# Kernel tuning notes

Measured on AMD Instinct MI355X. Metric: run time of the kernel, lower is better.

The kernel has to match this reference:

```python
import jax, jax.numpy as jnp
import numpy as np

KEEP_RATIO = 0.5
B, H, W = 8, 1024, 1024


def setup_inputs() -> dict:
    key = jax.random.key(0)
    k1, k2, k3 = jax.random.split(key, 3)
    logits = jax.random.normal(k1, (B, 1, H, W), dtype=jnp.float32)
    targets = jax.random.randint(k2, (B, 1, H, W), 0, 2, dtype=jnp.int32)
    tissue_mask = jax.random.randint(k3, (B, 1, H, W), 0, 2, dtype=jnp.int32)
    return {"logits": logits, "targets": targets, "tissue_mask": tissue_mask}


def reference(logits, targets, tissue_mask):
    b = logits.shape[0]
    x = logits.reshape(b, -1)                       # (B, N)
    t = targets.reshape(b, -1).astype(x.dtype)      # {0,1}
    m = tissue_mask.reshape(b, -1).astype(x.dtype)  # {0,1}
    n = x.shape[1]

    # stable binary_cross_entropy_with_logits, reduction='none'
    bce = jnp.maximum(x, 0.0) - x * t + jnp.log1p(jnp.exp(-jnp.abs(x)))
    loss = bce * m                                  # masked per-pixel loss

    pos = t * m                                     # positives inside tissue
    neg = (1.0 - t) * m                             # negatives inside tissue
    n_pos = jnp.sum(pos, axis=1)                    # (B,)
    n_neg = jnp.sum(neg, axis=1)

    k_all = max(1, int(n * KEEP_RATIO))             # static python int
    # kept count per row: all positives + top-(k_all - n_pos) negatives (clamped)
    k_keep = n_pos + jnp.minimum(jnp.maximum(k_all - n_pos, 0.0), n_neg)  # (B,)

    BIG = jnp.asarray(1e30, x.dtype)
    # sort key: positives always first, then negatives by loss, then non-tissue
    sort_key = jnp.where(pos > 0, BIG, jnp.where(neg > 0, loss, -BIG))
    order = jnp.argsort(-sort_key, axis=1)          # descending
    sorted_loss = jnp.take_along_axis(loss, order, axis=1)

    ranks = jnp.arange(n, dtype=x.dtype)
    keep = (ranks[None, :] < k_keep[:, None]).astype(x.dtype)
    per_sample = jnp.sum(sorted_loss * keep, axis=1) / jnp.maximum(k_keep, 1.0)
    # fallback when no tissue pixels at all: torch keeps index 0 (loss there is 0)
    per_sample = jnp.where(k_keep > 0, per_sample, loss[:, 0])
    return jnp.mean(per_sample)
```

## Files before the change

### kernel.cpp

```cpp
#include <hip/hip_runtime.h>
#include <cstdint>
#include <cstddef>

#define N_PIX   1048576
#define B_ROWS  8
#define K_ALL   524288
#define BLOCKS_PER_ROW 128
#define NSTAGE  8
#define NBINS   1024
#define FXSHIFT 11
#define NCOPY   8
#define CSHIFT  42
#define SUMMASK ((1ull << CSHIFT) - 1ull)
#define FPSCALE 262144.0f


__global__ __launch_bounds__(256) void k_pass1(
    const float4* __restrict__ lg, const int4* __restrict__ tg, const int4* __restrict__ mk,
    unsigned long long* __restrict__ hist,
    unsigned* __restrict__ partNpos, double* __restrict__ partSpos, float* __restrict__ out)
{
    __shared__ unsigned long long hq[NBINS];
    __shared__ unsigned swp[4];
    __shared__ double   sws[4];
    const int tid = threadIdx.x;

    for (int b = tid; b < NBINS; b += 256) hq[b] = 0ull;
    if (blockIdx.x == 0 && tid == 0) *out = 0.f;
    __syncthreads();
    __builtin_amdgcn_sched_barrier(0);

    const int r = blockIdx.x >> 7;
    const size_t qbase = (size_t)blockIdx.x * (NSTAGE * 256) + tid;

    unsigned npos = 0; float spos = 0.f;

    auto proc = [&](float xx, int tt, int mm) {
        float ax = fabsf(xx);
        float e = __expf(-ax);
        float l = __logf(1.f + e);
        float bce = fmaxf(xx, 0.f) - xx * (float)tt + l;
        if (mm) {
            if (tt) { npos++; spos += bce; }
            else {
                unsigned fx = (unsigned)__float2uint_rn(bce * FPSCALE);
                unsigned bin = fx >> FXSHIFT;
                if (bin >= NBINS) bin = NBINS - 1;
                atomicAdd(&hq[bin], (1ull << CSHIFT) | (unsigned long long)fx);
            }
        }
    };

    float4 x[2]; int4 t[2]; int4 m[2];
    x[0] = lg[qbase]; t[0] = tg[qbase]; m[0] = mk[qbase];
    #pragma unroll
    for (int j = 0; j < NSTAGE; ++j) {
        const int cur = j & 1, nxt = cur ^ 1;
        if (j < NSTAGE - 1) {
            const size_t q = qbase + (size_t)(j + 1) * 256;
            x[nxt] = lg[q]; t[nxt] = tg[q]; m[nxt] = mk[q];
        }
        __builtin_amdgcn_sched_barrier(0);
        proc(x[cur].x, t[cur].x, m[cur].x);
        proc(x[cur].y, t[cur].y, m[cur].y);
        proc(x[cur].z, t[cur].z, m[cur].z);
        proc(x[cur].w, t[cur].w, m[cur].w);
        __builtin_amdgcn_sched_barrier(0);
    }

    for (int o = 32; o; o >>= 1) {
        npos += __shfl_down(npos, o);
        spos += __shfl_down(spos, o);
    }
    if ((tid & 63) == 0) { swp[tid >> 6] = npos; sws[tid >> 6] = (double)spos; }
    __syncthreads();
    if (tid == 0) {
        partNpos[blockIdx.x] = swp[0] + swp[1] + swp[2] + swp[3];
        partSpos[blockIdx.x] = sws[0] + sws[1] + sws[2] + sws[3];
    }

    unsigned long long* gh = hist + ((size_t)r * NCOPY + (blockIdx.x & (NCOPY - 1))) * NBINS;
    for (int b = tid; b < NBINS; b += 256) {
        unsigned long long v = hq[b];
        if (v) atomicAdd(&gh[b], v);
    }
}

__global__ __launch_bounds__(256) void k_final(
    const unsigned long long* __restrict__ hist,
    const unsigned* __restrict__ partNpos, const double* __restrict__ partSpos,
    float* __restrict__ out)
{
    __shared__ unsigned sc[2][256];
    __shared__ double   sd[2][256];
    __shared__ unsigned swp[4];
    __shared__ double   sws[4];
    __shared__ unsigned rcntgt, rcnt1;
    __shared__ double rsumgt, rsum1;

    const int r = blockIdx.x, tid = threadIdx.x;
    const unsigned long long* gh = hist + (size_t)r * NCOPY * NBINS;
    const double inv = 1.0 / (double)FPSCALE;

    {
        unsigned np = (tid < BLOCKS_PER_ROW) ? partNpos[r * BLOCKS_PER_ROW + tid] : 0u;
        double   sp = (tid < BLOCKS_PER_ROW) ? partSpos[r * BLOCKS_PER_ROW + tid] : 0.0;
        for (int o = 32; o; o >>= 1) { np += __shfl_down(np, o); sp += __shfl_down(sp, o); }
        if ((tid & 63) == 0) { swp[tid >> 6] = np; sws[tid >> 6] = sp; }
    }
    __syncthreads();
    const unsigned npos = swp[0] + swp[1] + swp[2] + swp[3];
    const double sumPos = sws[0] + sws[1] + sws[2] + sws[3];
    __syncthreads();

    const int per = NBINS / 256;
    const int b0 = NBINS - 1 - tid * per;
    unsigned lc[4]; double lsum[4];
    unsigned pc = 0; double ps = 0.0;
    #pragma unroll
    for (int i = 0; i < per; ++i) {
        unsigned long long v = 0ull;
        #pragma unroll
        for (int c = 0; c < NCOPY; ++c) v += gh[(size_t)c * NBINS + (b0 - i)];
        lc[i] = (unsigned)(v >> CSHIFT);
        lsum[i] = (double)(v & SUMMASK) * inv;
        pc += lc[i]; ps += lsum[i];
    }

    int pp = 0;
    sc[0][tid] = pc; sd[0][tid] = ps;
    __syncthreads();
    for (int ofs = 1; ofs < 256; ofs <<= 1) {
        unsigned c = sc[pp][tid]; double s = sd[pp][tid];
        if (tid >= ofs) { c += sc[pp][tid - ofs]; s += sd[pp][tid - ofs]; }
        sc[pp ^ 1][tid] = c; sd[pp ^ 1][tid] = s;
        pp ^= 1;
        __syncthreads();
    }
    const unsigned nneg   = sc[pp][255];
    const double   sumNeg = sd[pp][255];

    long kl = (long)K_ALL - (long)npos;
    if (kl < 0) kl = 0;
    if (kl > (long)nneg) kl = (long)nneg;
    const unsigned Kneg = (unsigned)kl;

    double sum_sel = 0.0;
    if (Kneg >= nneg) {
        sum_sel = sumNeg;
    } else if (Kneg > 0) {
        unsigned inc = sc[pp][tid];
        unsigned exc = inc - pc;
        double   exs = sd[pp][tid] - ps;
        if (exc < Kneg && Kneg <= inc) {
            unsigned cum = exc; double csum = exs;
            #pragma unroll
            for (int i = 0; i < per; ++i) {
                if (cum + lc[i] >= Kneg) {
                    rcntgt = cum; rsumgt = csum;
                    rcnt1 = lc[i]; rsum1 = lsum[i];
                    break;
                }
                cum += lc[i]; csum += lsum[i];
            }
        }
        __syncthreads();
        if (tid == 0) {
            const unsigned cntT1 = rcnt1;
            const double   sumT1 = rsum1;
            const unsigned Kp = Kneg - rcntgt;
            const double w = 1.0 / 128.0;
            const double avg = sumT1 / (double)cntT1;
            const double topmean = avg + 0.5 * w * (1.0 - (double)Kp / (double)cntT1);
            sum_sel = rsumgt + (double)Kp * topmean;
        }
    }

    if (tid == 0) {
        unsigned long long kk = (unsigned long long)npos + (unsigned long long)Kneg;
        double per_s = 0.0;
        if (kk > 0) per_s = (sumPos + sum_sel) / (double)kk;
        atomicAdd(out, (float)(per_s / (double)B_ROWS));
    }
}

extern "C" void kernel_launch(void* const* d_in, const int* in_sizes, int n_in,
                              void* d_out, int out_size, void* d_ws, size_t ws_size,
                              hipStream_t stream)
{
    const float* logits = (const float*)d_in[0];
    const int*   targets = (const int*)d_in[1];
    const int*   tissue = (const int*)d_in[2];

    const int NBLK = B_ROWS * BLOCKS_PER_ROW;
    char* ws = (char*)d_ws;
    size_t off = 0;
    unsigned long long* hist = (unsigned long long*)(ws + off);
    off += (size_t)B_ROWS * NCOPY * NBINS * 8;
    size_t zero_size = off;
    unsigned* partNpos = (unsigned*)(ws + off); off += (size_t)NBLK * 4;
    double*   partSpos = (double*)(ws + off);   off += (size_t)NBLK * 8;

    hipMemsetAsync(ws, 0, zero_size, stream);

    k_pass1<<<NBLK, 256, 0, stream>>>(
        (const float4*)logits, (const int4*)targets, (const int4*)tissue,
        hist, partNpos, partSpos, (float*)d_out);
    k_final<<<B_ROWS, 256, 0, stream>>>(hist, partNpos, partSpos, (float*)d_out);
}
```

Measured before the change: 121.5 us.

## Split loss and histogram into separate kernels via packed 16-bit fixed-point buffer

The fused pass is split in two. One kernel computes BCE and writes each negative pixel's loss as a 16-bit fixed-point value (others get a sentinel), packed two per word, into a workspace buffer. A second kernel reads these values and builds the per-row shared-memory histogram with 64-bit atomics, then merges it into the global histogram copies. This separates the bandwidth-bound transcendental pass from the atomic-heavy histogram pass to raise occupancy in each, at the cost of an extra 16 MB write and read. Fixed-point precision also drops from a 2^18 to a 2^13 scale, with losses clamped at 0xFFFE, which coarsens the top-k boundary interpolation.

```diff
diff --git a/kernel.cpp b/kernel.cpp
--- a/kernel.cpp
+++ b/kernel.cpp
@@ -5,67 +5,63 @@
 #define N_PIX   1048576
 #define B_ROWS  8
 #define K_ALL   524288
-#define BLOCKS_PER_ROW 128
-#define NSTAGE  8
+#define LOSS_BLOCKS 2048
+#define LOSS_STAGES 4
+#define HIST_BLOCKS 1024
+#define HPT     4
 #define NBINS   1024
-#define FXSHIFT 11
 #define NCOPY   8
 #define CSHIFT  42
 #define SUMMASK ((1ull << CSHIFT) - 1ull)
-#define FPSCALE 262144.0f
-
-
-__global__ __launch_bounds__(256) void k_pass1(
+#define FXSCALE 8192.0f
+
+
+__global__ __launch_bounds__(256) void k_loss(
     const float4* __restrict__ lg, const int4* __restrict__ tg, const int4* __restrict__ mk,
-    unsigned long long* __restrict__ hist,
+    uint4* __restrict__ fxout,
     unsigned* __restrict__ partNpos, double* __restrict__ partSpos, float* __restrict__ out)
 {
-    __shared__ unsigned long long hq[NBINS];
     __shared__ unsigned swp[4];
     __shared__ double   sws[4];
     const int tid = threadIdx.x;
-
-    for (int b = tid; b < NBINS; b += 256) hq[b] = 0ull;
     if (blockIdx.x == 0 && tid == 0) *out = 0.f;
-    __syncthreads();
-    __builtin_amdgcn_sched_barrier(0);
-
-    const int r = blockIdx.x >> 7;
-    const size_t qbase = (size_t)blockIdx.x * (NSTAGE * 256) + tid;
+
+    const size_t qbase = (size_t)blockIdx.x * (LOSS_STAGES * 256) + tid;
 
     unsigned npos = 0; float spos = 0.f;
 
-    auto proc = [&](float xx, int tt, int mm) {
+    auto bcefx = [&](float xx, int tt, int mm) -> unsigned {
         float ax = fabsf(xx);
         float e = __expf(-ax);
         float l = __logf(1.f + e);
         float bce = fmaxf(xx, 0.f) - xx * (float)tt + l;
-        if (mm) {
-            if (tt) { npos++; spos += bce; }
-            else {
-                unsigned fx = (unsigned)__float2uint_rn(bce * FPSCALE);
-                unsigned bin = fx >> FXSHIFT;
-                if (bin >= NBINS) bin = NBINS - 1;
-                atomicAdd(&hq[bin], (1ull << CSHIFT) | (unsigned long long)fx);
-            }
-        }
+        unsigned fx = __float2uint_rn(bce * FXSCALE);
+        if (fx > 0xFFFEu) fx = 0xFFFEu;
+        if (mm && tt) { npos++; spos += bce; }
+        return (mm && !tt) ? fx : 0xFFFFu;
     };
 
     float4 x[2]; int4 t[2]; int4 m[2];
     x[0] = lg[qbase]; t[0] = tg[qbase]; m[0] = mk[qbase];
-    #pragma unroll
-    for (int j = 0; j < NSTAGE; ++j) {
+    uint4 acc;
+    #pragma unroll
+    for (int j = 0; j < LOSS_STAGES; ++j) {
         const int cur = j & 1, nxt = cur ^ 1;
-        if (j < NSTAGE - 1) {
+        if (j < LOSS_STAGES - 1) {
             const size_t q = qbase + (size_t)(j + 1) * 256;
             x[nxt] = lg[q]; t[nxt] = tg[q]; m[nxt] = mk[q];
         }
         __builtin_amdgcn_sched_barrier(0);
-        proc(x[cur].x, t[cur].x, m[cur].x);
-        proc(x[cur].y, t[cur].y, m[cur].y);
-        proc(x[cur].z, t[cur].z, m[cur].z);
-        proc(x[cur].w, t[cur].w, m[cur].w);
-        __builtin_amdgcn_sched_barrier(0);
+        unsigned f0 = bcefx(x[cur].x, t[cur].x, m[cur].x);
+        unsigned f1 = bcefx(x[cur].y, t[cur].y, m[cur].y);
+        unsigned f2 = bcefx(x[cur].z, t[cur].z, m[cur].z);
+        unsigned f3 = bcefx(x[cur].w, t[cur].w, m[cur].w);
+        if ((j & 1) == 0) {
+            acc.x = f0 | (f1 << 16); acc.y = f2 | (f3 << 16);
+        } else {
+            acc.z = f0 | (f1 << 16); acc.w = f2 | (f3 << 16);
+            fxout[(size_t)blockIdx.x * (2 * 256) + (size_t)(j >> 1) * 256 + tid] = acc;
+        }
     }
 
     for (int o = 32; o; o >>= 1) {
@@ -78,11 +74,41 @@
         partNpos[blockIdx.x] = swp[0] + swp[1] + swp[2] + swp[3];
         partSpos[blockIdx.x] = sws[0] + sws[1] + sws[2] + sws[3];
     }
+}
+
+__global__ __launch_bounds__(256) void k_hist(
+    const uint4* __restrict__ fx4, unsigned long long* __restrict__ hist)
+{
+    __shared__ unsigned long long hq[NBINS];
+    const int tid = threadIdx.x;
+    for (int b = tid; b < NBINS; b += 256) hq[b] = 0ull;
+    __syncthreads();
+
+    const int r = blockIdx.x >> 7;
+    const size_t base = (size_t)blockIdx.x * (HPT * 256) + tid;
+
+    uint4 v[HPT];
+    #pragma unroll
+    for (int s = 0; s < HPT; ++s) v[s] = fx4[base + (size_t)s * 256];
+
+    #pragma unroll
+    for (int s = 0; s < HPT; ++s) {
+        unsigned w[4] = { v[s].x, v[s].y, v[s].z, v[s].w };
+        #pragma unroll
+        for (int q = 0; q < 4; ++q) {
+            unsigned lo = w[q] & 0xFFFFu, hi = w[q] >> 16;
+            if (lo != 0xFFFFu)
+                atomicAdd(&hq[lo >> 6], (1ull << CSHIFT) | (unsigned long long)lo);
+            if (hi != 0xFFFFu)
+                atomicAdd(&hq[hi >> 6], (1ull << CSHIFT) | (unsigned long long)hi);
+        }
+    }
+    __syncthreads();
 
     unsigned long long* gh = hist + ((size_t)r * NCOPY + (blockIdx.x & (NCOPY - 1))) * NBINS;
     for (int b = tid; b < NBINS; b += 256) {
-        unsigned long long v = hq[b];
-        if (v) atomicAdd(&gh[b], v);
+        unsigned long long u = hq[b];
+        if (u) atomicAdd(&gh[b], u);
     }
 }
 
@@ -100,11 +126,11 @@
 
     const int r = blockIdx.x, tid = threadIdx.x;
     const unsigned long long* gh = hist + (size_t)r * NCOPY * NBINS;
-    const double inv = 1.0 / (double)FPSCALE;
+    const double inv = 1.0 / (double)FXSCALE;
 
     {
-        unsigned np = (tid < BLOCKS_PER_ROW) ? partNpos[r * BLOCKS_PER_ROW + tid] : 0u;
-        double   sp = (tid < BLOCKS_PER_ROW) ? partSpos[r * BLOCKS_PER_ROW + tid] : 0.0;
+        unsigned np = partNpos[r * 256 + tid];
+        double   sp = partSpos[r * 256 + tid];
         for (int o = 32; o; o >>= 1) { np += __shfl_down(np, o); sp += __shfl_down(sp, o); }
         if ((tid & 63) == 0) { swp[tid >> 6] = np; sws[tid >> 6] = sp; }
     }
@@ -192,19 +218,20 @@
     const int*   targets = (const int*)d_in[1];
     const int*   tissue = (const int*)d_in[2];
 
-    const int NBLK = B_ROWS * BLOCKS_PER_ROW;
     char* ws = (char*)d_ws;
     size_t off = 0;
     unsigned long long* hist = (unsigned long long*)(ws + off);
     off += (size_t)B_ROWS * NCOPY * NBINS * 8;
     size_t zero_size = off;
-    unsigned* partNpos = (unsigned*)(ws + off); off += (size_t)NBLK * 4;
-    double*   partSpos = (double*)(ws + off);   off += (size_t)NBLK * 8;
+    unsigned* partNpos = (unsigned*)(ws + off); off += (size_t)LOSS_BLOCKS * 4;
+    double*   partSpos = (double*)(ws + off);   off += (size_t)LOSS_BLOCKS * 8;
+    uint4*    fxout    = (uint4*)(ws + off);    off += (size_t)(B_ROWS * N_PIX / 8) * 16;
 
     hipMemsetAsync(ws, 0, zero_size, stream);
 
-    k_pass1<<<NBLK, 256, 0, stream>>>(
+    k_loss<<<LOSS_BLOCKS, 256, 0, stream>>>(
         (const float4*)logits, (const int4*)targets, (const int4*)tissue,
-        hist, partNpos, partSpos, (float*)d_out);
+        fxout, partNpos, partSpos, (float*)d_out);
+    k_hist<<<HIST_BLOCKS, 256, 0, stream>>>((const uint4*)fxout, hist);
     k_final<<<B_ROWS, 256, 0, stream>>>(hist, partNpos, partSpos, (float*)d_out);
 }
```

Measured after the change: 132.7 us. +9.3%, slower.

## Stage pass1 inputs through LDS with async global_load_lds triple buffering

Applied to the files above, without the earlier changes.

Replaces the register double-buffered loads in the first pass with direct global-to-LDS DMA (global_load_lds, 16 bytes per lane) into a three-slot ring, gated by vmcnt waits and barriers. It also halves the grid to 512 blocks, each covering 16384 pixels over 16 tiles, so more loads are in flight per block. The intent is to hide memory latency behind the BCE and histogram-atomic work. In exchange it adds about 36KB of LDS per block and two barriers per tile, and lowers the block count. That can reduce occupancy and the latency hiding that the LDS atomics depend on.

```diff
diff --git a/kernel.cpp b/kernel.cpp
--- a/kernel.cpp
+++ b/kernel.cpp
@@ -5,8 +5,12 @@
 #define N_PIX   1048576
 #define B_ROWS  8
 #define K_ALL   524288
-#define BLOCKS_PER_ROW 128
-#define NSTAGE  8
+#define NBLK1   512
+#define BLOCKS_PER_ROW 64
+#define PX_PER_BLOCK   16384
+#define NT      16
+#define TPX     1024
+#define NSLOT   3
 #define NBINS   1024
 #define FXSHIFT 11
 #define NCOPY   8
@@ -15,31 +19,47 @@
 #define FPSCALE 262144.0f
 
 
+typedef __attribute__((address_space(1))) const void gvoid_t;
+typedef __attribute__((address_space(3))) void lvoid_t;
+__device__ __forceinline__ void dma16(const void* g, void* l) {
+    __builtin_amdgcn_global_load_lds((gvoid_t*)g, (lvoid_t*)l, 16, 0, 0);
+}
+#define SBAR()  __builtin_amdgcn_s_barrier()
+#define SCHED() __builtin_amdgcn_sched_barrier(0)
+#define WAITV(N) asm volatile("s_waitcnt vmcnt(" #N ")" ::: "memory")
+
 __global__ __launch_bounds__(256) void k_pass1(
-    const float4* __restrict__ lg, const int4* __restrict__ tg, const int4* __restrict__ mk,
+    const float* __restrict__ lg, const int* __restrict__ tg, const int* __restrict__ mk,
     unsigned long long* __restrict__ hist,
     unsigned* __restrict__ partNpos, double* __restrict__ partSpos, float* __restrict__ out)
 {
+    __shared__ uint4 stage[NSLOT][3][TPX / 4];
     __shared__ unsigned long long hq[NBINS];
     __shared__ unsigned swp[4];
     __shared__ double   sws[4];
     const int tid = threadIdx.x;
+    const int w = tid >> 6, l = tid & 63;
 
     for (int b = tid; b < NBINS; b += 256) hq[b] = 0ull;
     if (blockIdx.x == 0 && tid == 0) *out = 0.f;
     __syncthreads();
-    __builtin_amdgcn_sched_barrier(0);
-
-    const int r = blockIdx.x >> 7;
-    const size_t qbase = (size_t)blockIdx.x * (NSTAGE * 256) + tid;
+
+    const size_t p0 = (size_t)blockIdx.x * PX_PER_BLOCK;
+
+    auto issue = [&](int j, int s) {
+        const size_t px = p0 + (size_t)j * TPX + (size_t)w * 256 + (size_t)l * 4;
+        dma16(lg + px, &stage[s][0][w * 64]);
+        dma16(tg + px, &stage[s][1][w * 64]);
+        dma16(mk + px, &stage[s][2][w * 64]);
+    };
 
     unsigned npos = 0; float spos = 0.f;
-
-    auto proc = [&](float xx, int tt, int mm) {
+    auto proc = [&](unsigned xu, unsigned tt, unsigned mm) {
+        float xx = __uint_as_float(xu);
         float ax = fabsf(xx);
-        float e = __expf(-ax);
-        float l = __logf(1.f + e);
-        float bce = fmaxf(xx, 0.f) - xx * (float)tt + l;
+        float e  = __expf(-ax);
+        float lo = __logf(1.f + e);
+        float bce = fmaxf(xx, 0.f) - xx * (float)tt + lo;
         if (mm) {
             if (tt) { npos++; spos += bce; }
             else {
@@ -51,22 +71,34 @@
         }
     };
 
-    float4 x[2]; int4 t[2]; int4 m[2];
-    x[0] = lg[qbase]; t[0] = tg[qbase]; m[0] = mk[qbase];
-    #pragma unroll
-    for (int j = 0; j < NSTAGE; ++j) {
-        const int cur = j & 1, nxt = cur ^ 1;
-        if (j < NSTAGE - 1) {
-            const size_t q = qbase + (size_t)(j + 1) * 256;
-            x[nxt] = lg[q]; t[nxt] = tg[q]; m[nxt] = mk[q];
-        }
-        __builtin_amdgcn_sched_barrier(0);
-        proc(x[cur].x, t[cur].x, m[cur].x);
-        proc(x[cur].y, t[cur].y, m[cur].y);
-        proc(x[cur].z, t[cur].z, m[cur].z);
-        proc(x[cur].w, t[cur].w, m[cur].w);
-        __builtin_amdgcn_sched_barrier(0);
-    }
+    auto consume = [&](int s) {
+        uint4 lv = stage[s][0][tid];
+        uint4 tv = stage[s][1][tid];
+        uint4 mv = stage[s][2][tid];
+        proc(lv.x, tv.x, mv.x);
+        proc(lv.y, tv.y, mv.y);
+        proc(lv.z, tv.z, mv.z);
+        proc(lv.w, tv.w, mv.w);
+    };
+
+    issue(0, 0); issue(1, 1); issue(2, 2);
+
+    int slot = 0;
+    #pragma unroll 1
+    for (int j = 0; j <= NT - 4; ++j) {
+        WAITV(6); SCHED();
+        SBAR();
+        consume(slot);
+        SCHED();
+        SBAR();
+        issue(j + 3, slot);
+        slot = (slot == NSLOT - 1) ? 0 : slot + 1;
+    }
+    WAITV(6); SCHED(); SBAR(); consume(slot); slot = (slot == NSLOT - 1) ? 0 : slot + 1;
+    WAITV(3); SCHED(); SBAR(); consume(slot); slot = (slot == NSLOT - 1) ? 0 : slot + 1;
+    WAITV(0); SCHED(); SBAR(); consume(slot);
+
+    __syncthreads();
 
     for (int o = 32; o; o >>= 1) {
         npos += __shfl_down(npos, o);
@@ -79,6 +111,7 @@
         partSpos[blockIdx.x] = sws[0] + sws[1] + sws[2] + sws[3];
     }
 
+    const int r = blockIdx.x >> 6;
     unsigned long long* gh = hist + ((size_t)r * NCOPY + (blockIdx.x & (NCOPY - 1))) * NBINS;
     for (int b = tid; b < NBINS; b += 256) {
         unsigned long long v = hq[b];
@@ -192,19 +225,17 @@
     const int*   targets = (const int*)d_in[1];
     const int*   tissue = (const int*)d_in[2];
 
-    const int NBLK = B_ROWS * BLOCKS_PER_ROW;
     char* ws = (char*)d_ws;
     size_t off = 0;
     unsigned long long* hist = (unsigned long long*)(ws + off);
     off += (size_t)B_ROWS * NCOPY * NBINS * 8;
     size_t zero_size = off;
-    unsigned* partNpos = (unsigned*)(ws + off); off += (size_t)NBLK * 4;
-    double*   partSpos = (double*)(ws + off);   off += (size_t)NBLK * 8;
+    unsigned* partNpos = (unsigned*)(ws + off); off += (size_t)NBLK1 * 4;
+    double*   partSpos = (double*)(ws + off);   off += (size_t)NBLK1 * 8;
 
     hipMemsetAsync(ws, 0, zero_size, stream);
 
-    k_pass1<<<NBLK, 256, 0, stream>>>(
-        (const float4*)logits, (const int4*)targets, (const int4*)tissue,
-        hist, partNpos, partSpos, (float*)d_out);
+    k_pass1<<<NBLK1, 256, 0, stream>>>(
+        logits, targets, tissue, hist, partNpos, partSpos, (float*)d_out);
     k_final<<<B_ROWS, 256, 0, stream>>>(hist, partNpos, partSpos, (float*)d_out);
 }
```

Result: slower. 125.4 us (+3.2%).
